# Kernel tuning notes

Measured on AMD Instinct MI355X. Metric: run time of the kernel, lower is better.

## Reference

```python
import jax, jax.numpy as jnp
import numpy as np

DZ, DA, K, T, BS, H = 32, 16, 3, 128, 512, 128


def setup_inputs() -> dict:
    key = jax.random.key(0)
    ks = jax.random.split(key, 8)
    s = 0.02
    # A/C: identity-like init (as in the torch module) plus small noise, per mixture k and timestep t
    A = jnp.eye(DZ, dtype=jnp.float32) + s * jax.random.normal(ks[0], (K, T, DZ, DZ), jnp.float32)
    C = jnp.eye(DA, DZ, dtype=jnp.float32) + s * jax.random.normal(ks[1], (K, T, DA, DZ), jnp.float32)
    a0 = jnp.zeros((DA,), jnp.float32)
    a = jax.random.normal(ks[2], (BS, T, DA), jnp.float32)

    def lw(k, shape):
        return 0.05 * jax.random.normal(k, shape, jnp.float32)

    Wih0 = lw(ks[3], (4 * H, DA)); Whh0 = lw(ks[4], (4 * H, H))
    bih0 = jnp.zeros((4 * H,), jnp.float32); bhh0 = jnp.zeros((4 * H,), jnp.float32)
    Wih1 = lw(ks[5], (4 * H, H)); Whh1 = lw(ks[6], (4 * H, H))
    bih1 = jnp.zeros((4 * H,), jnp.float32); bhh1 = jnp.zeros((4 * H,), jnp.float32)
    Wlin = lw(ks[7], (K, H)); blin = jnp.zeros((K,), jnp.float32)
    return dict(a=a, A=A, C=C, a0=a0, Wih0=Wih0, Whh0=Whh0, bih0=bih0, bhh0=bhh0,
                Wih1=Wih1, Whh1=Whh1, bih1=bih1, bhh1=bhh1, Wlin=Wlin, blin=blin)


def _lstm_layer(x, Wih, Whh, bih, bhh):
    # x: (bs, L, din) -> (bs, L, H); PyTorch gate order i, f, g, o; zero initial state
    Hd = Whh.shape[1]
    b = bih + bhh

    def step(carry, xt):
        h, c = carry
        g = xt @ Wih.T + h @ Whh.T + b
        i, f, gg, o = jnp.split(g, 4, axis=-1)
        c = jax.nn.sigmoid(f) * c + jax.nn.sigmoid(i) * jnp.tanh(gg)
        h = jax.nn.sigmoid(o) * jnp.tanh(c)
        return (h, c), h

    h0 = jnp.zeros((x.shape[0], Hd), x.dtype)
    _, hs = jax.lax.scan(step, (h0, h0), jnp.swapaxes(x, 0, 1))
    return jnp.swapaxes(hs, 0, 1)


def _filter(a, A, C, a0, Wih0, Whh0, bih0, bhh0, Wih1, Whh1, bih1, bhh1, Wlin, blin):
    bs, L, da = a.shape
    dz = A.shape[-1]
    R = 0.01 * jnp.eye(da, dtype=a.dtype)
    Q = 0.01 * jnp.eye(dz, dtype=a.dtype)

    # dynamics network: alpha_t from [a_0, a_0..a_{L-2}]
    code = jnp.concatenate([jnp.broadcast_to(a0, (bs, 1, da)), a[:, :-1]], axis=1)
    h = _lstm_layer(code, Wih0, Whh0, bih0, bhh0)
    h = _lstm_layer(h, Wih1, Whh1, bih1, bhh1)
    alpha = jax.nn.softmax(h @ Wlin.T + blin, axis=-1)  # (bs, L, K)

    A_mix = jnp.einsum('blk,klij->blij', alpha, A)  # (bs, L, dz, dz)
    C_mix = jnp.einsum('blk,klij->blij', alpha, C)  # (bs, L, da, dz)
    # A is applied at index t+1 for the prediction step; last slot is a dummy (its output is unused)
    A_next = jnp.concatenate([A_mix[:, 1:], A_mix[:, -1:]], axis=1)

    mu0 = jnp.zeros((bs, dz), a.dtype)
    sig0 = jnp.broadcast_to(jnp.eye(dz, dtype=a.dtype), (bs, dz, dz))
    I = jnp.eye(dz, dtype=a.dtype)

    def step(carry, inp):
        mu_pred, sigma_pred = carry
        Ct, At_next, at = inp  # (bs,da,dz), (bs,dz,dz), (bs,da)
        r = at - jnp.einsum('bij,bj->bi', Ct, mu_pred)
        CtT = jnp.swapaxes(Ct, 1, 2)
        S = Ct @ sigma_pred @ CtT + R                      # (bs, da, da)
        Kg = sigma_pred @ CtT @ jnp.linalg.inv(S)          # (bs, dz, da)
        mu = mu_pred + jnp.einsum('bij,bj->bi', Kg, r)
        sigma = (I - Kg @ Ct) @ sigma_pred
        mu_next = jnp.einsum('bij,bj->bi', At_next, mu)
        sigma_next = At_next @ sigma @ jnp.swapaxes(At_next, 1, 2) + Q
        return (mu_next, sigma_next), mu

    xs = (jnp.swapaxes(C_mix, 0, 1), jnp.swapaxes(A_next, 0, 1), jnp.swapaxes(a, 0, 1))
    _, means = jax.lax.scan(step, (mu0, sig0), xs)
    return jnp.swapaxes(means, 0, 1)  # filtered means (bs, L, dz)


def reference(a, A, C, a0, Wih0, Whh0, bih0, bhh0, Wih1, Whh1, bih1, bhh1, Wlin, blin):
    return _filter(a, A, C, a0, Wih0, Whh0, bih0, bhh0,
                   Wih1, Whh1, bih1, bhh1, Wlin, blin)
```

## Files before the change

kernel.cpp:

```cpp
#include <hip/hip_runtime.h>
#include <hip/hip_fp16.h>
#include <cstdint>

#define T_LEN 128
#define DA    16
#define DZ    32
#define HH    128

__device__ __forceinline__ float sigm(float x){ return 1.0f/(1.0f + __expf(-x)); }
__device__ __forceinline__ float tanh_f(float x){ return 1.0f - 2.0f/(__expf(2.0f*x)+1.0f); }
__device__ __forceinline__ float dot4(float4 a, float4 b){ return a.x*b.x + a.y*b.y + a.z*b.z + a.w*b.w; }

typedef _Float16 h2v __attribute__((ext_vector_type(2)));
__device__ __forceinline__ float fdot2(uint32_t w, uint32_t h, float acc){
  union{uint32_t u; h2v v;} a, b; a.u = w; b.u = h;
  return __builtin_amdgcn_fdot2(a.v, b.v, acc, false);
}
__device__ __forceinline__ uint32_t packh2(float x, float y){
  return (uint32_t)__half_as_ushort(__float2half(x)) |
         ((uint32_t)__half_as_ushort(__float2half(y)) << 16);
}
__device__ __forceinline__ float h2lo(uint32_t u){
  return __half2float(__ushort_as_half((unsigned short)(u & 0xffffu)));
}
__device__ __forceinline__ float h2hi(uint32_t u){
  return __half2float(__ushort_as_half((unsigned short)(u >> 16)));
}
__device__ __forceinline__ float dot8(uint4 a, uint4 b, float acc){
  acc = fdot2(a.x, b.x, acc); acc = fdot2(a.y, b.y, acc);
  acc = fdot2(a.z, b.z, acc); acc = fdot2(a.w, b.w, acc);
  return acc;
}
__device__ __forceinline__ float dot8f(uint4 h, float4 f0, float4 f1, float acc){
  acc += h2lo(h.x)*f0.x + h2hi(h.x)*f0.y + h2lo(h.y)*f0.z + h2hi(h.y)*f0.w;
  acc += h2lo(h.z)*f1.x + h2hi(h.z)*f1.y + h2lo(h.w)*f1.z + h2hi(h.w)*f1.w;
  return acc;
}

#define BAR() do { asm volatile("s_waitcnt lgkmcnt(0)" ::: "memory"); \
                   __builtin_amdgcn_s_barrier(); } while (0)

__global__ void prep_kernel(const float* __restrict__ Wih0, const float* __restrict__ Whh0,
                            const float* __restrict__ bih0, const float* __restrict__ bhh0,
                            const float* __restrict__ Wih1, const float* __restrict__ Whh1,
                            const float* __restrict__ bih1, const float* __restrict__ bhh1,
                            uint32_t* __restrict__ ws) {
  int idx = blockIdx.x*256 + threadIdx.x;
  if (idx < 4096) {
    int q = idx & 3, g = (idx >> 2) & 511, m = idx >> 11;
    int k0 = 8*m + 2*q;
    ws[idx] = packh2(Wih0[g*DA + k0], Wih0[g*DA + k0 + 1]);
  } else if (idx < 36864) {
    int f = idx - 4096;
    int q = f & 3, g = (f >> 2) & 511, m = f >> 11;
    int k0 = 8*m + 2*q;
    ws[idx] = packh2(Whh0[g*HH + k0], Whh0[g*HH + k0 + 1]);
  } else if (idx < 69632) {
    int f = idx - 36864;
    int q = f & 3, g = (f >> 2) & 511, m = f >> 11;
    int k0 = 8*m + 2*q;
    ws[idx] = packh2(Wih1[g*HH + k0], Wih1[g*HH + k0 + 1]);
  } else if (idx < 102400) {
    int f = idx - 69632;
    int q = f & 3, g = (f >> 2) & 511, m = f >> 11;
    int k0 = 8*m + 2*q;
    ws[idx] = packh2(Whh1[g*HH + k0], Whh1[g*HH + k0 + 1]);
  } else if (idx < 102912) {
    int j = idx - 102400;
    ((float*)ws)[idx] = bih0[j] + bhh0[j];
  } else if (idx < 103424) {
    int j = idx - 102912;
    ((float*)ws)[idx] = bih1[j] + bhh1[j];
  }
}

__global__ __launch_bounds__(512, 2) void lstm_kernel(
    const float* __restrict__ a, const float* __restrict__ a0,
    const uint32_t* __restrict__ wsw, const float* __restrict__ Wlin,
    const float* __restrict__ blin, float* __restrict__ alpha_out) {
  const uint4* Wih0p = (const uint4*)(wsw);
  const uint4* Whh0p = (const uint4*)(wsw + 4096);
  const uint4* Wih1p = (const uint4*)(wsw + 36864);
  const uint4* Whh1p = (const uint4*)(wsw + 69632);
  const float* b0v = (const float*)(wsw + 102400);
  const float* b1v = (const float*)(wsw + 102912);

  __shared__ __align__(16) uint32_t sxh[2][T_LEN][8];
  __shared__ __align__(16) uint32_t sh0h[2][64];
  __shared__ __align__(16) uint32_t sh1h[2][64];
  __shared__ float gates[2][4*HH];

  int tid = threadIdx.x;
  int lane = tid & 63;
  int wv = tid >> 6;
  int bb = blockIdx.x * 2;

  uint4 wi0[2], wh0[16], wi1[16], wh1[16];
  #pragma unroll
  for (int m = 0; m < 2; ++m)  wi0[m] = Wih0p[m*512 + tid];
  #pragma unroll
  for (int m = 0; m < 16; ++m) wh0[m] = Whh0p[m*512 + tid];
  #pragma unroll
  for (int m = 0; m < 16; ++m) wi1[m] = Wih1p[m*512 + tid];
  #pragma unroll
  for (int m = 0; m < 16; ++m) wh1[m] = Whh1p[m*512 + tid];
  float bi0 = b0v[tid], bi1 = b1v[tid];

  for (int i = tid; i < 2*T_LEN*8; i += 512) {
    int r = i / (T_LEN*8), rem = i % (T_LEN*8), t = rem >> 3, p = rem & 7;
    float x0, x1;
    if (t == 0) { x0 = a0[2*p]; x1 = a0[2*p+1]; }
    else {
      const float* src = a + ((size_t)(bb + r)*T_LEN + (t-1))*DA;
      x0 = src[2*p]; x1 = src[2*p+1];
    }
    sxh[r][t][p] = packh2(x0, x1);
  }
  float wl00 = Wlin[0*HH + 2*lane], wl01 = Wlin[0*HH + 2*lane+1];
  float wl10 = Wlin[1*HH + 2*lane], wl11 = Wlin[1*HH + 2*lane+1];
  float wl20 = Wlin[2*HH + 2*lane], wl21 = Wlin[2*HH + 2*lane+1];
  float bl0 = blin[0], bl1 = blin[1], bl2 = blin[2];
  float cl0 = 0.f, cl1 = 0.f;
  if (tid < 128) { sh0h[wv][lane] = 0u; sh1h[wv][lane] = 0u; }
  __syncthreads();

  #pragma unroll 1
  for (int t = 0; t < T_LEN; ++t) {
    {
      float g0a = bi0, g0b = 0.f, g1a = bi0, g1b = 0.f;
      uint4 xA0 = *(const uint4*)&sxh[0][t][0];
      uint4 xA1 = *(const uint4*)&sxh[0][t][4];
      uint4 xB0 = *(const uint4*)&sxh[1][t][0];
      uint4 xB1 = *(const uint4*)&sxh[1][t][4];
      g0a = fdot2(wi0[0].x, xA0.x, g0a); g0b = fdot2(wi0[0].y, xA0.y, g0b);
      g0a = fdot2(wi0[0].z, xA0.z, g0a); g0b = fdot2(wi0[0].w, xA0.w, g0b);
      g0a = fdot2(wi0[1].x, xA1.x, g0a); g0b = fdot2(wi0[1].y, xA1.y, g0b);
      g0a = fdot2(wi0[1].z, xA1.z, g0a); g0b = fdot2(wi0[1].w, xA1.w, g0b);
      g1a = fdot2(wi0[0].x, xB0.x, g1a); g1b = fdot2(wi0[0].y, xB0.y, g1b);
      g1a = fdot2(wi0[0].z, xB0.z, g1a); g1b = fdot2(wi0[0].w, xB0.w, g1b);
      g1a = fdot2(wi0[1].x, xB1.x, g1a); g1b = fdot2(wi0[1].y, xB1.y, g1b);
      g1a = fdot2(wi0[1].z, xB1.z, g1a); g1b = fdot2(wi0[1].w, xB1.w, g1b);
      #pragma unroll
      for (int m = 0; m < 16; ++m) {
        uint4 w = wh0[m];
        uint4 hA = *(const uint4*)&sh0h[0][4*m];
        uint4 hB = *(const uint4*)&sh0h[1][4*m];
        g0a = fdot2(w.x, hA.x, g0a); g0b = fdot2(w.y, hA.y, g0b);
        g0a = fdot2(w.z, hA.z, g0a); g0b = fdot2(w.w, hA.w, g0b);
        g1a = fdot2(w.x, hB.x, g1a); g1b = fdot2(w.y, hB.y, g1b);
        g1a = fdot2(w.z, hB.z, g1a); g1b = fdot2(w.w, hB.w, g1b);
      }
      gates[0][tid] = g0a + g0b;
      gates[1][tid] = g1a + g1b;
    }
    __syncthreads();
    if (tid < 256) {
      int row = tid >> 7, cell = tid & 127;
      float iv = gates[row][cell],      fv = gates[row][cell+HH],
            qv = gates[row][cell+2*HH], ov = gates[row][cell+3*HH];
      cl0 = sigm(fv)*cl0 + sigm(iv)*tanh_f(qv);
      float hv = sigm(ov)*tanh_f(cl0);
      ((__half*)&sh0h[0][0])[row*128 + cell] = __float2half(hv);
    }
    __syncthreads();
    {
      float g0a = bi1, g0b = 0.f, g1a = bi1, g1b = 0.f;
      #pragma unroll
      for (int m = 0; m < 16; ++m) {
        uint4 w = wi1[m];
        uint4 hA = *(const uint4*)&sh0h[0][4*m];
        uint4 hB = *(const uint4*)&sh0h[1][4*m];
        g0a = fdot2(w.x, hA.x, g0a); g0b = fdot2(w.y, hA.y, g0b);
        g0a = fdot2(w.z, hA.z, g0a); g0b = fdot2(w.w, hA.w, g0b);
        g1a = fdot2(w.x, hB.x, g1a); g1b = fdot2(w.y, hB.y, g1b);
        g1a = fdot2(w.z, hB.z, g1a); g1b = fdot2(w.w, hB.w, g1b);
      }
      #pragma unroll
      for (int m = 0; m < 16; ++m) {
        uint4 w = wh1[m];
        uint4 hA = *(const uint4*)&sh1h[0][4*m];
        uint4 hB = *(const uint4*)&sh1h[1][4*m];
        g0a = fdot2(w.x, hA.x, g0a); g0b = fdot2(w.y, hA.y, g0b);
        g0a = fdot2(w.z, hA.z, g0a); g0b = fdot2(w.w, hA.w, g0b);
        g1a = fdot2(w.x, hB.x, g1a); g1b = fdot2(w.y, hB.y, g1b);
        g1a = fdot2(w.z, hB.z, g1a); g1b = fdot2(w.w, hB.w, g1b);
      }
      gates[0][tid] = g0a + g0b;
      gates[1][tid] = g1a + g1b;
    }
    __syncthreads();
    if (tid < 256) {
      int row = tid >> 7, cell = tid & 127;
      float iv = gates[row][cell],      fv = gates[row][cell+HH],
            qv = gates[row][cell+2*HH], ov = gates[row][cell+3*HH];
      cl1 = sigm(fv)*cl1 + sigm(iv)*tanh_f(qv);
      float hv = sigm(ov)*tanh_f(cl1);
      ((__half*)&sh1h[0][0])[row*128 + cell] = __float2half(hv);
    }
    __syncthreads();
    if (tid < 128) {
      uint32_t hw = sh1h[wv][lane];
      float hv0 = h2lo(hw), hv1 = h2hi(hw);
      float p0 = hv0*wl00 + hv1*wl01;
      float p1 = hv0*wl10 + hv1*wl11;
      float p2 = hv0*wl20 + hv1*wl21;
      #pragma unroll
      for (int off = 32; off > 0; off >>= 1) {
        p0 += __shfl_down(p0, off); p1 += __shfl_down(p1, off); p2 += __shfl_down(p2, off);
      }
      if (lane == 0) {
        float l0 = p0 + bl0, l1 = p1 + bl1, l2 = p2 + bl2;
        float mx = fmaxf(l0, fmaxf(l1, l2));
        float e0=__expf(l0-mx), e1=__expf(l1-mx), e2=__expf(l2-mx);
        float inv = 1.0f/(e0+e1+e2);
        float* dst = alpha_out + (((size_t)(bb+wv))*T_LEN + t)*3;
        dst[0]=e0*inv; dst[1]=e1*inv; dst[2]=e2*inv;
      }
    }
  }
}

__global__ __launch_bounds__(256) void kalman_kernel(
    const float* __restrict__ a, const float* __restrict__ A,
    const float* __restrict__ C, const float* __restrict__ alpha,
    float* __restrict__ out) {
  __shared__ __align__(16) uint32_t SgH[DZ][20];
  __shared__ __align__(16) uint32_t AmH[DZ][20];
  __shared__ __align__(16) uint32_t Sp2H[DZ][20];
  __shared__ __align__(16) uint32_t T2H[DZ][20];
  __shared__ __align__(16) uint32_t CmH[DA][20];
  __shared__ __align__(16) uint32_t NnTH[DA][20];
  __shared__ __align__(16) uint32_t NnH[DZ][12];
  __shared__ __align__(16) uint32_t KgH[DZ][12];
  __shared__ __align__(16) uint32_t SinvH[DA][12];
  __shared__ __align__(16) float Aug[DA][36];
  __shared__ __align__(16) float sa[T_LEN][DA];
  __shared__ float salpha[T_LEN*3];
  __shared__ __align__(16) float muvF[DZ], munF[DZ], rv[DA];

  int tid = threadIdx.x;
  int b = blockIdx.x;

  for (int e = tid; e < T_LEN*DA; e += 256) (&sa[0][0])[e] = a[(size_t)b*T_LEN*DA + e];
  for (int e = tid; e < T_LEN*3; e += 256) salpha[e] = alpha[(size_t)b*T_LEN*3 + e];
  __syncthreads();

  const int i8 = tid >> 3, jq = tid & 7;
  const int i32 = tid & 31, g = tid >> 5;
  const int j2 = g * 2, j4 = g * 4;

  {
    uint2 iv;
    iv.x = packh2((i8==4*jq  )?1.f:0.f, (i8==4*jq+1)?1.f:0.f);
    iv.y = packh2((i8==4*jq+2)?1.f:0.f, (i8==4*jq+3)?1.f:0.f);
    *(uint2*)&SgH[i8][jq*2] = iv;
    if (tid < DZ) muvF[tid] = 0.0f;
  }

  const float4* A4 = (const float4*)A;
  const float4* C4 = (const float4*)C;
  float4 pA0 = A4[(0*T_LEN + 1)*256 + tid];
  float4 pA1 = A4[(1*T_LEN + 1)*256 + tid];
  float4 pA2 = A4[(2*T_LEN + 1)*256 + tid];
  float4 pC0, pC1, pC2;
  if (tid < 128) {
    pC0 = C4[(0*T_LEN + 0)*128 + tid];
    pC1 = C4[(1*T_LEN + 0)*128 + tid];
    pC2 = C4[(2*T_LEN + 0)*128 + tid];
  }
  __syncthreads();

  #pragma unroll 1
  for (int t = 0; t < T_LEN; ++t) {
    int ta = (t < T_LEN-1) ? t+1 : t;
    float b10 = salpha[ta*3+0], b11 = salpha[ta*3+1], b12 = salpha[ta*3+2];
    float b00 = salpha[t*3+0],  b01 = salpha[t*3+1],  b02 = salpha[t*3+2];

    {
      float vx = b10*pA0.x + b11*pA1.x + b12*pA2.x;
      float vy = b10*pA0.y + b11*pA1.y + b12*pA2.y;
      float vz = b10*pA0.z + b11*pA1.z + b12*pA2.z;
      float vw = b10*pA0.w + b11*pA1.w + b12*pA2.w;
      uint2 pv; pv.x = packh2(vx, vy); pv.y = packh2(vz, vw);
      *(uint2*)&AmH[i8][jq*2] = pv;
      if (tid < 128) {
        float cx = b00*pC0.x + b01*pC1.x + b02*pC2.x;
        float cy = b00*pC0.y + b01*pC1.y + b02*pC2.y;
        float cz = b00*pC0.z + b01*pC1.z + b02*pC2.z;
        float cw = b00*pC0.w + b01*pC1.w + b02*pC2.w;
        uint2 pc; pc.x = packh2(cx, cy); pc.y = packh2(cz, cw);
        *(uint2*)&CmH[tid>>3][(tid&7)*2] = pc;
      }
      int tn  = (t+1 < T_LEN) ? t+1 : T_LEN-1;
      int tan = (tn < T_LEN-1) ? tn+1 : tn;
      pA0 = A4[(0*T_LEN + tan)*256 + tid];
      pA1 = A4[(1*T_LEN + tan)*256 + tid];
      pA2 = A4[(2*T_LEN + tan)*256 + tid];
      if (tid < 128) {
        pC0 = C4[(0*T_LEN + tn)*128 + tid];
        pC1 = C4[(1*T_LEN + tn)*128 + tid];
        pC2 = C4[(2*T_LEN + tn)*128 + tid];
      }
    }
    BAR();

    {
      uint4 s0 = *(const uint4*)&SgH[i32][0];
      uint4 s1 = *(const uint4*)&SgH[i32][4];
      uint4 s2 = *(const uint4*)&SgH[i32][8];
      uint4 s3 = *(const uint4*)&SgH[i32][12];
      uint4 cA0 = *(const uint4*)&CmH[j2][0];
      uint4 cA1 = *(const uint4*)&CmH[j2][4];
      uint4 cA2 = *(const uint4*)&CmH[j2][8];
      uint4 cA3 = *(const uint4*)&CmH[j2][12];
      uint4 cB0 = *(const uint4*)&CmH[j2+1][0];
      uint4 cB1 = *(const uint4*)&CmH[j2+1][4];
      uint4 cB2 = *(const uint4*)&CmH[j2+1][8];
      uint4 cB3 = *(const uint4*)&CmH[j2+1][12];
      float aA = dot8(s3,cA3, dot8(s2,cA2, dot8(s1,cA1, dot8(s0,cA0, 0.f))));
      float aB = dot8(s3,cB3, dot8(s2,cB2, dot8(s1,cB1, dot8(s0,cB0, 0.f))));
      NnH[i32][g] = packh2(aA, aB);
      __half* ntp = (__half*)&NnTH[0][0];
      ntp[j2*40 + i32]     = __float2half(aA);
      ntp[(j2+1)*40 + i32] = __float2half(aB);
    }
    BAR();

    {
      int i = tid & 15, j = tid >> 4;
      uint4 c0 = *(const uint4*)&CmH[i][0];
      uint4 c1 = *(const uint4*)&CmH[i][4];
      uint4 c2 = *(const uint4*)&CmH[i][8];
      uint4 c3 = *(const uint4*)&CmH[i][12];
      uint4 n0 = *(const uint4*)&NnTH[j][0];
      uint4 n1 = *(const uint4*)&NnTH[j][4];
      uint4 n2 = *(const uint4*)&NnTH[j][8];
      uint4 n3 = *(const uint4*)&NnTH[j][12];
      float s = dot8(c3,n3, dot8(c2,n2, dot8(c1,n1, dot8(c0,n0, 0.f))));
      Aug[i][j] = s + ((i == j) ? 0.01f : 0.0f);
      Aug[i][16 + j] = (i == j) ? 1.0f : 0.0f;
    }
    BAR();

    if (tid < 64) {
      int lane = tid;
      int r = lane >> 2, cb = lane & 3;
      float v[8];
      #pragma unroll
      for (int j = 0; j < 8; ++j) v[j] = Aug[r][cb*8 + j];
      #define GJ_PIVOT(P, CTRL)                                                \
      {                                                                        \
        float App = __int_as_float(__builtin_amdgcn_readlane(                  \
                      __float_as_int(v[(P) & 7]), ((P) << 2) | ((P) >> 3)));   \
        float fv  = __int_as_float(__builtin_amdgcn_mov_dpp(                   \
                      __float_as_int(v[(P) & 7]), (CTRL), 0xf, 0xf, true));    \
        float prow[8];                                                         \
        _Pragma("unroll")                                                      \
        for (int j = 0; j < 8; ++j) prow[j] = __shfl(v[j], ((P) << 2) | cb, 64); \
        float pinv = 1.0f / App;                                               \
        if (r == (P)) {                                                        \
          _Pragma("unroll")                                                    \
          for (int j = 0; j < 8; ++j) v[j] *= pinv;                            \
        } else {                                                               \
          float fp = fv * pinv;                                                \
          _Pragma("unroll")                                                    \
          for (int j = 0; j < 8; ++j) v[j] -= fp * prow[j];                    \
        }                                                                      \
      }
      GJ_PIVOT(0, 0x00)  GJ_PIVOT(1, 0x00)  GJ_PIVOT(2, 0x00)  GJ_PIVOT(3, 0x00)
      GJ_PIVOT(4, 0x00)  GJ_PIVOT(5, 0x00)  GJ_PIVOT(6, 0x00)  GJ_PIVOT(7, 0x00)
      GJ_PIVOT(8, 0x55)  GJ_PIVOT(9, 0x55)  GJ_PIVOT(10, 0x55) GJ_PIVOT(11, 0x55)
      GJ_PIVOT(12, 0x55) GJ_PIVOT(13, 0x55) GJ_PIVOT(14, 0x55) GJ_PIVOT(15, 0x55)
      #undef GJ_PIVOT
      if (cb >= 2) {
        uint4 w;
        w.x = packh2(v[0], v[1]); w.y = packh2(v[2], v[3]);
        w.z = packh2(v[4], v[5]); w.w = packh2(v[6], v[7]);
        *(uint4*)&SinvH[r][(cb-2)*4] = w;
      }
    } else if (tid < 64 + DA) {
      int j = tid - 64;
      uint4 c0 = *(const uint4*)&CmH[j][0];
      uint4 c1 = *(const uint4*)&CmH[j][4];
      uint4 c2 = *(const uint4*)&CmH[j][8];
      uint4 c3 = *(const uint4*)&CmH[j][12];
      const float4* mv = (const float4*)muvF;
      float4 m0 = mv[0], m1 = mv[1], m2 = mv[2], m3 = mv[3];
      float4 m4 = mv[4], m5 = mv[5], m6 = mv[6], m7 = mv[7];
      float d = 0.f;
      d = dot8f(c0, m0, m1, d);
      d = dot8f(c1, m2, m3, d);
      d = dot8f(c2, m4, m5, d);
      d = dot8f(c3, m6, m7, d);
      rv[j] = sa[t][j] - d;
    }
    BAR();

    {
      uint4 n0 = *(const uint4*)&NnH[i32][0];
      uint4 n1 = *(const uint4*)&NnH[i32][4];
      uint4 sA0 = *(const uint4*)&SinvH[j2][0];
      uint4 sA1 = *(const uint4*)&SinvH[j2][4];
      uint4 sB0 = *(const uint4*)&SinvH[j2+1][0];
      uint4 sB1 = *(const uint4*)&SinvH[j2+1][4];
      float aA = dot8(n1, sA1, dot8(n0, sA0, 0.f));
      float aB = dot8(n1, sB1, dot8(n0, sB0, 0.f));
      KgH[i32][g] = packh2(aA, aB);
    }
    BAR();

    {
      uint4 k0 = *(const uint4*)&KgH[i32][0];
      uint4 k1 = *(const uint4*)&KgH[i32][4];
      float acc[4];
      #pragma unroll
      for (int c = 0; c < 4; ++c) {
        uint4 b0 = *(const uint4*)&NnH[j4+c][0];
        uint4 b1 = *(const uint4*)&NnH[j4+c][4];
        acc[c] = dot8(k1, b1, dot8(k0, b0, 0.f));
      }
      uint2 sgp = *(const uint2*)&SgH[i32][g*2];
      uint2 o;
      o.x = packh2(h2lo(sgp.x) - acc[0], h2hi(sgp.x) - acc[1]);
      o.y = packh2(h2lo(sgp.y) - acc[2], h2hi(sgp.y) - acc[3]);
      *(uint2*)&Sp2H[i32][g*2] = o;
    }
    if (tid >= 128 && tid < 128 + DZ) {
      int q = tid - 128;
      uint4 k0 = *(const uint4*)&KgH[q][0];
      uint4 k1 = *(const uint4*)&KgH[q][4];
      const float4* rp = (const float4*)rv;
      float4 r0 = rp[0], r1 = rp[1], r2 = rp[2], r3 = rp[3];
      float m = muvF[q];
      m = dot8f(k0, r0, r1, m);
      m = dot8f(k1, r2, r3, m);
      munF[q] = m;
      out[((size_t)b*T_LEN + t)*DZ + q] = m;
    }
    BAR();

    {
      uint4 a0 = *(const uint4*)&AmH[i32][0];
      uint4 a1 = *(const uint4*)&AmH[i32][4];
      uint4 a2 = *(const uint4*)&AmH[i32][8];
      uint4 a3 = *(const uint4*)&AmH[i32][12];
      float acc[4];
      #pragma unroll
      for (int c = 0; c < 4; ++c) {
        uint4 p0 = *(const uint4*)&Sp2H[j4+c][0];
        uint4 p1 = *(const uint4*)&Sp2H[j4+c][4];
        uint4 p2 = *(const uint4*)&Sp2H[j4+c][8];
        uint4 p3 = *(const uint4*)&Sp2H[j4+c][12];
        acc[c] = dot8(a3,p3, dot8(a2,p2, dot8(a1,p1, dot8(a0,p0, 0.f))));
      }
      uint2 o; o.x = packh2(acc[0], acc[1]); o.y = packh2(acc[2], acc[3]);
      *(uint2*)&T2H[i32][g*2] = o;
    }
    BAR();

    {
      uint4 t0 = *(const uint4*)&T2H[i32][0];
      uint4 t1 = *(const uint4*)&T2H[i32][4];
      uint4 t2 = *(const uint4*)&T2H[i32][8];
      uint4 t3 = *(const uint4*)&T2H[i32][12];
      float acc[4];
      #pragma unroll
      for (int c = 0; c < 4; ++c) {
        uint4 a0 = *(const uint4*)&AmH[j4+c][0];
        uint4 a1 = *(const uint4*)&AmH[j4+c][4];
        uint4 a2 = *(const uint4*)&AmH[j4+c][8];
        uint4 a3 = *(const uint4*)&AmH[j4+c][12];
        acc[c] = dot8(t3,a3, dot8(t2,a2, dot8(t1,a1, dot8(t0,a0, 0.f))));
        if (i32 == j4 + c) acc[c] += 0.01f;
      }
      uint2 o; o.x = packh2(acc[0], acc[1]); o.y = packh2(acc[2], acc[3]);
      *(uint2*)&SgH[i32][g*2] = o;
    }
    if (tid >= 128 && tid < 128 + DZ) {
      int q = tid - 128;
      uint4 a0 = *(const uint4*)&AmH[q][0];
      uint4 a1 = *(const uint4*)&AmH[q][4];
      uint4 a2 = *(const uint4*)&AmH[q][8];
      uint4 a3 = *(const uint4*)&AmH[q][12];
      const float4* mp = (const float4*)munF;
      float4 n0 = mp[0], n1 = mp[1], n2 = mp[2], n3 = mp[3];
      float4 n4 = mp[4], n5 = mp[5], n6 = mp[6], n7 = mp[7];
      float m = 0.f;
      m = dot8f(a0, n0, n1, m);
      m = dot8f(a1, n2, n3, m);
      m = dot8f(a2, n4, n5, m);
      m = dot8f(a3, n6, n7, m);
      muvF[q] = m;
    }
    BAR();
  }
}

extern "C" void kernel_launch(void* const* d_in, const int* in_sizes, int n_in,
                              void* d_out, int out_size, void* d_ws, size_t ws_size,
                              hipStream_t stream) {
  const float* a    = (const float*)d_in[0];
  const float* A    = (const float*)d_in[1];
  const float* C    = (const float*)d_in[2];
  const float* a0   = (const float*)d_in[3];
  const float* Wih0 = (const float*)d_in[4];
  const float* Whh0 = (const float*)d_in[5];
  const float* bih0 = (const float*)d_in[6];
  const float* bhh0 = (const float*)d_in[7];
  const float* Wih1 = (const float*)d_in[8];
  const float* Whh1 = (const float*)d_in[9];
  const float* bih1 = (const float*)d_in[10];
  const float* bhh1 = (const float*)d_in[11];
  const float* Wlin = (const float*)d_in[12];
  const float* blin = (const float*)d_in[13];
  uint32_t* ws = (uint32_t*)d_ws;
  float* alpha = (float*)(ws + 103424);
  float* out = (float*)d_out;

  prep_kernel<<<404, 256, 0, stream>>>(Wih0, Whh0, bih0, bhh0, Wih1, Whh1, bih1, bhh1, ws);
  lstm_kernel<<<256, 512, 0, stream>>>(a, a0, ws, Wlin, blin, alpha);
  kalman_kernel<<<512, 256, 0, stream>>>(a, A, C, alpha, out);
}
```

Measured before the change: 1.068 ms.

## Remove per-step barriers by double-buffering Kalman mixes and deferring LSTM softmax

In the LSTM kernel, the output-head reduction is folded into the layer-1 cell update. Per-wave partials go to shared memory and the softmax for step t-1 is done by spare threads during the next step, which removes one __syncthreads per timestep. In the Kalman kernel, the mixed A/C matrices are double-buffered. The mix and prefetch for the next step run at the end of the current step, which removes one barrier per step. The cost is more shared memory and more complex indexing.

Measured after the change: 1.048 ms. About the same (-1.9%).

```diff
diff --git a/kernel.cpp b/kernel.cpp
--- a/kernel.cpp
+++ b/kernel.cpp
@@ -9,7 +9,6 @@
 
 __device__ __forceinline__ float sigm(float x){ return 1.0f/(1.0f + __expf(-x)); }
 __device__ __forceinline__ float tanh_f(float x){ return 1.0f - 2.0f/(__expf(2.0f*x)+1.0f); }
-__device__ __forceinline__ float dot4(float4 a, float4 b){ return a.x*b.x + a.y*b.y + a.z*b.z + a.w*b.w; }
 
 typedef _Float16 h2v __attribute__((ext_vector_type(2)));
 __device__ __forceinline__ float fdot2(uint32_t w, uint32_t h, float acc){
@@ -89,6 +88,7 @@
   __shared__ __align__(16) uint32_t sh0h[2][64];
   __shared__ __align__(16) uint32_t sh1h[2][64];
   __shared__ float gates[2][4*HH];
+  __shared__ float hpart[4][3];
 
   int tid = threadIdx.x;
   int lane = tid & 63;
@@ -116,9 +116,9 @@
     }
     sxh[r][t][p] = packh2(x0, x1);
   }
-  float wl00 = Wlin[0*HH + 2*lane], wl01 = Wlin[0*HH + 2*lane+1];
-  float wl10 = Wlin[1*HH + 2*lane], wl11 = Wlin[1*HH + 2*lane+1];
-  float wl20 = Wlin[2*HH + 2*lane], wl21 = Wlin[2*HH + 2*lane+1];
+  float wl0 = Wlin[0*HH + (tid & 127)];
+  float wl1 = Wlin[1*HH + (tid & 127)];
+  float wl2 = Wlin[2*HH + (tid & 127)];
   float bl0 = blin[0], bl1 = blin[1], bl2 = blin[2];
   float cl0 = 0.f, cl1 = 0.f;
   if (tid < 128) { sh0h[wv][lane] = 0u; sh1h[wv][lane] = 0u; }
@@ -154,6 +154,17 @@
       gates[1][tid] = g1a + g1b;
     }
     __syncthreads();
+    if (t > 0 && tid >= 504 && tid < 506) {
+      int row = tid - 504;
+      float l0 = hpart[2*row][0] + hpart[2*row+1][0] + bl0;
+      float l1 = hpart[2*row][1] + hpart[2*row+1][1] + bl1;
+      float l2 = hpart[2*row][2] + hpart[2*row+1][2] + bl2;
+      float mx = fmaxf(l0, fmaxf(l1, l2));
+      float e0=__expf(l0-mx), e1=__expf(l1-mx), e2=__expf(l2-mx);
+      float inv = 1.0f/(e0+e1+e2);
+      float* dst = alpha_out + (((size_t)(bb+row))*T_LEN + (t-1))*3;
+      dst[0]=e0*inv; dst[1]=e1*inv; dst[2]=e2*inv;
+    }
     if (tid < 256) {
       int row = tid >> 7, cell = tid & 127;
       float iv = gates[row][cell],      fv = gates[row][cell+HH],
@@ -196,27 +207,28 @@
       cl1 = sigm(fv)*cl1 + sigm(iv)*tanh_f(qv);
       float hv = sigm(ov)*tanh_f(cl1);
       ((__half*)&sh1h[0][0])[row*128 + cell] = __float2half(hv);
-    }
-    __syncthreads();
-    if (tid < 128) {
-      uint32_t hw = sh1h[wv][lane];
-      float hv0 = h2lo(hw), hv1 = h2hi(hw);
-      float p0 = hv0*wl00 + hv1*wl01;
-      float p1 = hv0*wl10 + hv1*wl11;
-      float p2 = hv0*wl20 + hv1*wl21;
+      float p0 = hv*wl0, p1 = hv*wl1, p2 = hv*wl2;
       #pragma unroll
       for (int off = 32; off > 0; off >>= 1) {
         p0 += __shfl_down(p0, off); p1 += __shfl_down(p1, off); p2 += __shfl_down(p2, off);
       }
       if (lane == 0) {
-        float l0 = p0 + bl0, l1 = p1 + bl1, l2 = p2 + bl2;
-        float mx = fmaxf(l0, fmaxf(l1, l2));
-        float e0=__expf(l0-mx), e1=__expf(l1-mx), e2=__expf(l2-mx);
-        float inv = 1.0f/(e0+e1+e2);
-        float* dst = alpha_out + (((size_t)(bb+wv))*T_LEN + t)*3;
-        dst[0]=e0*inv; dst[1]=e1*inv; dst[2]=e2*inv;
-      }
-    }
+        int w4 = tid >> 6;
+        hpart[w4][0] = p0; hpart[w4][1] = p1; hpart[w4][2] = p2;
+      }
+    }
+  }
+  __syncthreads();
+  if (tid >= 504 && tid < 506) {
+    int row = tid - 504;
+    float l0 = hpart[2*row][0] + hpart[2*row+1][0] + bl0;
+    float l1 = hpart[2*row][1] + hpart[2*row+1][1] + bl1;
+    float l2 = hpart[2*row][2] + hpart[2*row+1][2] + bl2;
+    float mx = fmaxf(l0, fmaxf(l1, l2));
+    float e0=__expf(l0-mx), e1=__expf(l1-mx), e2=__expf(l2-mx);
+    float inv = 1.0f/(e0+e1+e2);
+    float* dst = alpha_out + (((size_t)(bb+row))*T_LEN + (T_LEN-1))*3;
+    dst[0]=e0*inv; dst[1]=e1*inv; dst[2]=e2*inv;
   }
 }
 
@@ -225,10 +237,10 @@
     const float* __restrict__ C, const float* __restrict__ alpha,
     float* __restrict__ out) {
   __shared__ __align__(16) uint32_t SgH[DZ][20];
-  __shared__ __align__(16) uint32_t AmH[DZ][20];
+  __shared__ __align__(16) uint32_t AmH[2][DZ][20];
+  __shared__ __align__(16) uint32_t CmH[2][DA][20];
   __shared__ __align__(16) uint32_t Sp2H[DZ][20];
   __shared__ __align__(16) uint32_t T2H[DZ][20];
-  __shared__ __align__(16) uint32_t CmH[DA][20];
   __shared__ __align__(16) uint32_t NnTH[DA][20];
   __shared__ __align__(16) uint32_t NnH[DZ][12];
   __shared__ __align__(16) uint32_t KgH[DZ][12];
@@ -268,55 +280,57 @@
     pC1 = C4[(1*T_LEN + 0)*128 + tid];
     pC2 = C4[(2*T_LEN + 0)*128 + tid];
   }
+  #define MIX_AND_PREFETCH(bf, s, sn)                                          \
+  {                                                                            \
+    int ta_ = ((s) < T_LEN-1) ? (s)+1 : (s);                                   \
+    float bA0 = salpha[ta_*3+0], bA1 = salpha[ta_*3+1], bA2 = salpha[ta_*3+2]; \
+    float bC0 = salpha[(s)*3+0], bC1 = salpha[(s)*3+1], bC2 = salpha[(s)*3+2]; \
+    float vx = bA0*pA0.x + bA1*pA1.x + bA2*pA2.x;                              \
+    float vy = bA0*pA0.y + bA1*pA1.y + bA2*pA2.y;                              \
+    float vz = bA0*pA0.z + bA1*pA1.z + bA2*pA2.z;                              \
+    float vw = bA0*pA0.w + bA1*pA1.w + bA2*pA2.w;                              \
+    uint2 pv; pv.x = packh2(vx, vy); pv.y = packh2(vz, vw);                    \
+    *(uint2*)&AmH[bf][i8][jq*2] = pv;                                          \
+    if (tid < 128) {                                                           \
+      float cx = bC0*pC0.x + bC1*pC1.x + bC2*pC2.x;                            \
+      float cy = bC0*pC0.y + bC1*pC1.y + bC2*pC2.y;                            \
+      float cz = bC0*pC0.z + bC1*pC1.z + bC2*pC2.z;                            \
+      float cw = bC0*pC0.w + bC1*pC1.w + bC2*pC2.w;                            \
+      uint2 pc; pc.x = packh2(cx, cy); pc.y = packh2(cz, cw);                  \
+      *(uint2*)&CmH[bf][tid>>3][(tid&7)*2] = pc;                               \
+    }                                                                          \
+    int sn_ = ((sn) < T_LEN) ? (sn) : T_LEN-1;                                 \
+    int tan_ = (sn_ < T_LEN-1) ? sn_+1 : sn_;                                  \
+    pA0 = A4[(0*T_LEN + tan_)*256 + tid];                                      \
+    pA1 = A4[(1*T_LEN + tan_)*256 + tid];                                      \
+    pA2 = A4[(2*T_LEN + tan_)*256 + tid];                                      \
+    if (tid < 128) {                                                           \
+      pC0 = C4[(0*T_LEN + sn_)*128 + tid];                                     \
+      pC1 = C4[(1*T_LEN + sn_)*128 + tid];                                     \
+      pC2 = C4[(2*T_LEN + sn_)*128 + tid];                                     \
+    }                                                                          \
+  }
+
+  MIX_AND_PREFETCH(0, 0, 1)
   __syncthreads();
 
   #pragma unroll 1
   for (int t = 0; t < T_LEN; ++t) {
-    int ta = (t < T_LEN-1) ? t+1 : t;
-    float b10 = salpha[ta*3+0], b11 = salpha[ta*3+1], b12 = salpha[ta*3+2];
-    float b00 = salpha[t*3+0],  b01 = salpha[t*3+1],  b02 = salpha[t*3+2];
-
-    {
-      float vx = b10*pA0.x + b11*pA1.x + b12*pA2.x;
-      float vy = b10*pA0.y + b11*pA1.y + b12*pA2.y;
-      float vz = b10*pA0.z + b11*pA1.z + b12*pA2.z;
-      float vw = b10*pA0.w + b11*pA1.w + b12*pA2.w;
-      uint2 pv; pv.x = packh2(vx, vy); pv.y = packh2(vz, vw);
-      *(uint2*)&AmH[i8][jq*2] = pv;
-      if (tid < 128) {
-        float cx = b00*pC0.x + b01*pC1.x + b02*pC2.x;
-        float cy = b00*pC0.y + b01*pC1.y + b02*pC2.y;
-        float cz = b00*pC0.z + b01*pC1.z + b02*pC2.z;
-        float cw = b00*pC0.w + b01*pC1.w + b02*pC2.w;
-        uint2 pc; pc.x = packh2(cx, cy); pc.y = packh2(cz, cw);
-        *(uint2*)&CmH[tid>>3][(tid&7)*2] = pc;
-      }
-      int tn  = (t+1 < T_LEN) ? t+1 : T_LEN-1;
-      int tan = (tn < T_LEN-1) ? tn+1 : tn;
-      pA0 = A4[(0*T_LEN + tan)*256 + tid];
-      pA1 = A4[(1*T_LEN + tan)*256 + tid];
-      pA2 = A4[(2*T_LEN + tan)*256 + tid];
-      if (tid < 128) {
-        pC0 = C4[(0*T_LEN + tn)*128 + tid];
-        pC1 = C4[(1*T_LEN + tn)*128 + tid];
-        pC2 = C4[(2*T_LEN + tn)*128 + tid];
-      }
-    }
-    BAR();
+    const int p = t & 1;
 
     {
       uint4 s0 = *(const uint4*)&SgH[i32][0];
       uint4 s1 = *(const uint4*)&SgH[i32][4];
       uint4 s2 = *(const uint4*)&SgH[i32][8];
       uint4 s3 = *(const uint4*)&SgH[i32][12];
-      uint4 cA0 = *(const uint4*)&CmH[j2][0];
-      uint4 cA1 = *(const uint4*)&CmH[j2][4];
-      uint4 cA2 = *(const uint4*)&CmH[j2][8];
-      uint4 cA3 = *(const uint4*)&CmH[j2][12];
-      uint4 cB0 = *(const uint4*)&CmH[j2+1][0];
-      uint4 cB1 = *(const uint4*)&CmH[j2+1][4];
-      uint4 cB2 = *(const uint4*)&CmH[j2+1][8];
-      uint4 cB3 = *(const uint4*)&CmH[j2+1][12];
+      uint4 cA0 = *(const uint4*)&CmH[p][j2][0];
+      uint4 cA1 = *(const uint4*)&CmH[p][j2][4];
+      uint4 cA2 = *(const uint4*)&CmH[p][j2][8];
+      uint4 cA3 = *(const uint4*)&CmH[p][j2][12];
+      uint4 cB0 = *(const uint4*)&CmH[p][j2+1][0];
+      uint4 cB1 = *(const uint4*)&CmH[p][j2+1][4];
+      uint4 cB2 = *(const uint4*)&CmH[p][j2+1][8];
+      uint4 cB3 = *(const uint4*)&CmH[p][j2+1][12];
       float aA = dot8(s3,cA3, dot8(s2,cA2, dot8(s1,cA1, dot8(s0,cA0, 0.f))));
       float aB = dot8(s3,cB3, dot8(s2,cB2, dot8(s1,cB1, dot8(s0,cB0, 0.f))));
       NnH[i32][g] = packh2(aA, aB);
@@ -328,10 +342,10 @@
 
     {
       int i = tid & 15, j = tid >> 4;
-      uint4 c0 = *(const uint4*)&CmH[i][0];
-      uint4 c1 = *(const uint4*)&CmH[i][4];
-      uint4 c2 = *(const uint4*)&CmH[i][8];
-      uint4 c3 = *(const uint4*)&CmH[i][12];
+      uint4 c0 = *(const uint4*)&CmH[p][i][0];
+      uint4 c1 = *(const uint4*)&CmH[p][i][4];
+      uint4 c2 = *(const uint4*)&CmH[p][i][8];
+      uint4 c3 = *(const uint4*)&CmH[p][i][12];
       uint4 n0 = *(const uint4*)&NnTH[j][0];
       uint4 n1 = *(const uint4*)&NnTH[j][4];
       uint4 n2 = *(const uint4*)&NnTH[j][8];
@@ -380,10 +394,10 @@
       }
     } else if (tid < 64 + DA) {
       int j = tid - 64;
-      uint4 c0 = *(const uint4*)&CmH[j][0];
-      uint4 c1 = *(const uint4*)&CmH[j][4];
-      uint4 c2 = *(const uint4*)&CmH[j][8];
-      uint4 c3 = *(const uint4*)&CmH[j][12];
+      uint4 c0 = *(const uint4*)&CmH[p][j][0];
+      uint4 c1 = *(const uint4*)&CmH[p][j][4];
+      uint4 c2 = *(const uint4*)&CmH[p][j][8];
+      uint4 c3 = *(const uint4*)&CmH[p][j][12];
       const float4* mv = (const float4*)muvF;
       float4 m0 = mv[0], m1 = mv[1], m2 = mv[2], m3 = mv[3];
       float4 m4 = mv[4], m5 = mv[5], m6 = mv[6], m7 = mv[7];
@@ -440,10 +454,10 @@
     BAR();
 
     {
-      uint4 a0 = *(const uint4*)&AmH[i32][0];
-      uint4 a1 = *(const uint4*)&AmH[i32][4];
-      uint4 a2 = *(const uint4*)&AmH[i32][8];
-      uint4 a3 = *(const uint4*)&AmH[i32][12];
+      uint4 a0 = *(const uint4*)&AmH[p][i32][0];
+      uint4 a1 = *(const uint4*)&AmH[p][i32][4];
+      uint4 a2 = *(const uint4*)&AmH[p][i32][8];
+      uint4 a3 = *(const uint4*)&AmH[p][i32][12];
       float acc[4];
       #pragma unroll
       for (int c = 0; c < 4; ++c) {
@@ -466,10 +480,10 @@
       float acc[4];
       #pragma unroll
       for (int c = 0; c < 4; ++c) {
-        uint4 a0 = *(const uint4*)&AmH[j4+c][0];
-        uint4 a1 = *(const uint4*)&AmH[j4+c][4];
-        uint4 a2 = *(const uint4*)&AmH[j4+c][8];
-        uint4 a3 = *(const uint4*)&AmH[j4+c][12];
+        uint4 a0 = *(const uint4*)&AmH[p][j4+c][0];
+        uint4 a1 = *(const uint4*)&AmH[p][j4+c][4];
+        uint4 a2 = *(const uint4*)&AmH[p][j4+c][8];
+        uint4 a3 = *(const uint4*)&AmH[p][j4+c][12];
         acc[c] = dot8(t3,a3, dot8(t2,a2, dot8(t1,a1, dot8(t0,a0, 0.f))));
         if (i32 == j4 + c) acc[c] += 0.01f;
       }
@@ -478,10 +492,10 @@
     }
     if (tid >= 128 && tid < 128 + DZ) {
       int q = tid - 128;
-      uint4 a0 = *(const uint4*)&AmH[q][0];
-      uint4 a1 = *(const uint4*)&AmH[q][4];
-      uint4 a2 = *(const uint4*)&AmH[q][8];
-      uint4 a3 = *(const uint4*)&AmH[q][12];
+      uint4 a0 = *(const uint4*)&AmH[p][q][0];
+      uint4 a1 = *(const uint4*)&AmH[p][q][4];
+      uint4 a2 = *(const uint4*)&AmH[p][q][8];
+      uint4 a3 = *(const uint4*)&AmH[p][q][12];
       const float4* mp = (const float4*)munF;
       float4 n0 = mp[0], n1 = mp[1], n2 = mp[2], n3 = mp[3];
       float4 n4 = mp[4], n5 = mp[5], n6 = mp[6], n7 = mp[7];
@@ -492,8 +506,13 @@
       m = dot8f(a3, n6, n7, m);
       muvF[q] = m;
     }
-    BAR();
-  }
+    {
+      int s = (t+1 < T_LEN) ? t+1 : T_LEN-1;
+      MIX_AND_PREFETCH(p^1, s, t+2)
+    }
+    BAR();
+  }
+  #undef MIX_AND_PREFETCH
 }
 
 extern "C" void kernel_launch(void* const* d_in, const int* in_sizes, int n_in,
```
